# Kernel optimization log

Measured on AMD Instinct MI355X. Metric: run time of the kernel, lower is better.

Reference implementation:

```python
import jax, jax.numpy as jnp
import numpy as np

B = 512        # graphs per batch
N_NODES = 64   # nodes per graph
IN_CH = 256
EMBED = 64
TOPK = 20
NEG_SLOPE = 0.2


def setup_inputs() -> dict:
    key = jax.random.key(0)
    ks = jax.random.split(key, 6)
    N = B * N_NODES
    x = jax.random.normal(ks[0], (N, IN_CH), dtype=jnp.float32)
    # fully-connected graph WITH self loops, per graph, sorted source-major
    src = jnp.repeat(jnp.arange(N_NODES, dtype=jnp.int32), N_NODES)  # [n*n]
    dst = jnp.tile(jnp.arange(N_NODES, dtype=jnp.int32), N_NODES)    # [n*n]
    offs = (jnp.arange(B, dtype=jnp.int32) * N_NODES)[:, None]       # [B,1]
    l = (src[None, :] + offs).reshape(-1)
    r = (dst[None, :] + offs).reshape(-1)
    edge_index = jnp.stack([l, r]).astype(jnp.int32)                 # [2, B*n*n]
    batch = jnp.repeat(jnp.arange(B, dtype=jnp.int32), N_NODES)      # [N]
    glorot = lambda k, sh: jax.random.uniform(k, sh, jnp.float32,
                                              -1.0, 1.0) * np.sqrt(6.0 / (sh[0] + sh[-1]))
    Wl = glorot(ks[1], (EMBED, IN_CH))
    bl = jnp.zeros((EMBED,), jnp.float32)
    Wr = glorot(ks[2], (EMBED, IN_CH))
    br = jnp.zeros((EMBED,), jnp.float32)
    att = glorot(ks[3], (1, EMBED))
    return {"x": x, "edge_index": edge_index, "batch": batch,
            "Wl": Wl, "bl": bl, "Wr": Wr, "br": br, "att": att}


def reference(x, edge_index, batch, Wl, bl, Wr, br, att):
    N = x.shape[0]
    x_l = x @ Wl.T + bl                      # [N, D]
    x_r = x @ Wr.T + br                      # [N, D]
    l, r = edge_index[0], edge_index[1]
    # edge gather + GAT-style score
    e = jax.nn.leaky_relu(x_l[l] + x_r[r], negative_slope=NEG_SLOPE)  # [E, D]
    alpha = (e * att[0]).sum(axis=-1)                                  # [E]
    # segment softmax grouped by source node l (each group is non-empty)
    m = jax.ops.segment_max(alpha, l, num_segments=N)
    a = jnp.exp(alpha - m[l])
    s = jax.ops.segment_sum(a, l, num_segments=N)
    a = a / s[l]
    # kNN sparsify: zero the diagonal then per-row topk
    a3 = a.reshape(B, N_NODES, N_NODES)
    a3 = a3 * (1.0 - jnp.eye(N_NODES, dtype=a3.dtype))
    attention, indices = jax.lax.top_k(a3, TOPK)     # [B, n, k] sorted desc
    attention = attention.reshape(-1)                 # [B*n*k]
    offs = (jnp.arange(B, dtype=jnp.int32) * N_NODES)[:, None]
    index_i = (jnp.repeat(jnp.arange(N_NODES, dtype=jnp.int32), TOPK)[None, :]
               + offs).reshape(-1)
    index_j = (indices.astype(jnp.int32)
               + (jnp.arange(B, dtype=jnp.int32) * N_NODES)[:, None, None]).reshape(-1)
    new_edge_index = jnp.stack([index_i, index_j])    # [2, B*n*k]
    return new_edge_index, attention
```

## Files before the change

kernel.cpp:

```cpp
#include <hip/hip_runtime.h>
#include <stdint.h>

#define NGRAPH 512
#define NN 64
#define INCH 256
#define TOPK 20
#define EPR 655360

typedef __attribute__((ext_vector_type(8))) short bf16x8;
typedef __attribute__((ext_vector_type(4))) float f32x4;

#define STG   0
#define XLF   0
#define XRF   4352
#define ALF   8704
#define SLOF  13056
#define SROF  13120
#define ATTO  13184
#define SMEM_DW 13248

static __device__ __forceinline__ uint32_t f2bfbits(float f) {
  uint32_t u = __float_as_uint(f);
  return (u + 0x7FFFu + ((u >> 16) & 1u)) >> 16;
}
static __device__ __forceinline__ uint32_t pk2(float a, float b) {
  return f2bfbits(a) | (f2bfbits(b) << 16);
}

__global__ __launch_bounds__(256) void wpack(const float* __restrict__ Wl,
                                             const float* __restrict__ Wr,
                                             uint32_t* __restrict__ ws) {
  const int t = blockIdx.x * 256 + threadIdx.x;
  const float* src = (t < 8192) ? Wl : Wr;
  const int p = t & 8191;
  float2 v = *(const float2*)(src + (size_t)p * 2);
  ws[t] = pk2(v.x, v.y);
}

__global__ __launch_bounds__(1024, 8) void gat_fused(
    const float* __restrict__ x,
    const uint32_t* __restrict__ ws,
    const float* __restrict__ blv,
    const float* __restrict__ brv,
    const float* __restrict__ att,
    float* __restrict__ out)
{
  __shared__ __align__(16) uint32_t smemU[SMEM_DW];
  float* smemF = (float*)smemU;

  const int b    = blockIdx.x;
  const int t    = threadIdx.x;
  const int w    = t >> 6;
  const int lane = t & 63;
  const int quad = lane >> 4;
  const int lo   = lane & 15;
  const int nodeBase = b * NN;

  if (t < 64) smemF[ATTO + t] = att[t];

  const int half = w >> 3;
  const int r0   = ((w >> 1) & 3) * 16;
  const int kh   = w & 1;
  const int pair = w >> 1;

  f32x4 acc[4];
  #pragma unroll
  for (int ct = 0; ct < 4; ++ct) acc[ct] = (f32x4){0.f, 0.f, 0.f, 0.f};

  const uint4* wsV = (const uint4*)ws;
  #pragma unroll
  for (int ksl = 0; ksl < 4; ++ksl) {
    const int ks = kh * 4 + ksl;
    const int k0 = ks * 32 + quad * 8;
    const float* ap = x + (size_t)(nodeBase + r0 + lo) * INCH + k0;
    float4 a0 = *(const float4*)ap;
    float4 a1 = *(const float4*)(ap + 4);
    uint4 au = { pk2(a0.x, a0.y), pk2(a0.z, a0.w), pk2(a1.x, a1.y), pk2(a1.z, a1.w) };
    bf16x8 afrag = __builtin_bit_cast(bf16x8, au);
    #pragma unroll
    for (int ct = 0; ct < 4; ++ct) {
      const int n = ct * 16 + lo;
      uint4 bu = wsV[half * 2048 + n * 32 + ks * 4 + quad];
      bf16x8 bfrag = __builtin_bit_cast(bf16x8, bu);
      acc[ct] = __builtin_amdgcn_mfma_f32_16x16x32_bf16(afrag, bfrag, acc[ct], 0, 0, 0);
    }
  }

  if (kh) {
    #pragma unroll
    for (int ct = 0; ct < 4; ++ct)
      *(f32x4*)&smemF[STG + pair * 1280 + (ct * 16 + lo) * 20 + quad * 4] = acc[ct];
  }
  __syncthreads();

  f32x4 vfin[4];
  if (!kh) {
    const float* bias = half ? brv : blv;
    #pragma unroll
    for (int ct = 0; ct < 4; ++ct) {
      f32x4 pv = *(const f32x4*)&smemF[STG + pair * 1280 + (ct * 16 + lo) * 20 + quad * 4];
      const float bb = bias[ct * 16 + lo];
      vfin[ct][0] = acc[ct][0] + pv[0] + bb;
      vfin[ct][1] = acc[ct][1] + pv[1] + bb;
      vfin[ct][2] = acc[ct][2] + pv[2] + bb;
      vfin[ct][3] = acc[ct][3] + pv[3] + bb;
    }
  }
  __syncthreads();
  if (!kh) {
    const int dstBase = half ? XRF : XLF;
    #pragma unroll
    for (int ct = 0; ct < 4; ++ct)
      *(f32x4*)&smemF[dstBase + (ct * 16 + lo) * 68 + r0 + quad * 4] = vfin[ct];
  }
  __syncthreads();

  {
    const int idx = t >> 3;
    const int seg = t & 7;
    const int i = idx & 63;
    const int srcB = (idx < 64) ? XLF : XRF;
    float s = 0.f;
    #pragma unroll
    for (int dd = 0; dd < 8; ++dd) {
      const int d = dd * 8 + seg;
      s = fmaf(smemF[ATTO + d], smemF[srcB + d * 68 + i], s);
    }
    s += __shfl_xor(s, 1);
    s += __shfl_xor(s, 2);
    s += __shfl_xor(s, 4);
    if (seg == 0) smemF[((idx < 64) ? SLOF : SROF) + i] = s;
  }
  __syncthreads();

  {
    const int i0 = t >> 4;
    const int j0 = (t & 15) * 4;
    float pacc[4] = {0.f, 0.f, 0.f, 0.f};
    #pragma unroll 4
    for (int d = 0; d < 64; ++d) {
      const float xl0 = smemF[XLF + d * 68 + i0];
      const f32x4 xr  = *(const f32x4*)&smemF[XRF + d * 68 + j0];
      const float ad  = smemF[ATTO + d];
      #pragma unroll
      for (int c = 0; c < 4; ++c) {
        const float s0 = xl0 + xr[c];
        pacc[c] = fmaf(ad, fabsf(s0), pacc[c]);
      }
    }
    const float sl = smemF[SLOF + i0];
    const f32x4 srv = *(const f32x4*)&smemF[SROF + j0];
    f32x4 v;
    #pragma unroll
    for (int c = 0; c < 4; ++c)
      v[c] = 0.6f * (sl + srv[c]) + 0.4f * pacc[c];
    *(f32x4*)&smemF[ALF + i0 * 68 + j0] = v;
  }
  __syncthreads();

  {
    const int rB = w * 4;
    float aq[4], mq[4], Sq[4];
    uint32_t key[4];
    #pragma unroll
    for (int q = 0; q < 4; ++q)
      aq[q] = smemF[ALF + (rB + q) * 68 + lane];

    #pragma unroll
    for (int q = 0; q < 4; ++q) mq[q] = aq[q];
    #pragma unroll
    for (int msk = 32; msk >= 1; msk >>= 1)
      #pragma unroll
      for (int q = 0; q < 4; ++q)
        mq[q] = fmaxf(mq[q], __shfl_xor(mq[q], msk));

    #pragma unroll
    for (int q = 0; q < 4; ++q) Sq[q] = __expf(aq[q] - mq[q]);
    #pragma unroll
    for (int msk = 32; msk >= 1; msk >>= 1)
      #pragma unroll
      for (int q = 0; q < 4; ++q)
        Sq[q] += __shfl_xor(Sq[q], msk);

    #pragma unroll
    for (int q = 0; q < 4; ++q) {
      const uint32_t u = __float_as_uint(aq[q]);
      uint32_t kk = u ^ ((uint32_t)((int32_t)u >> 31) | 0x80000000u);
      kk = (kk & 0xFFFFFFC0u) | (uint32_t)(63 - lane);
      key[q] = (lane == rB + q) ? 0u : kk;
    }

    #pragma unroll
    for (int k = 2; k <= 64; k <<= 1) {
      #pragma unroll
      for (int j = k >> 1; j >= 1; j >>= 1) {
        const bool keep_max = (((lane & k) == 0) == ((lane & j) == 0));
        #pragma unroll
        for (int q = 0; q < 4; ++q) {
          const uint32_t p = __shfl_xor(key[q], j);
          const uint32_t mx = (key[q] > p) ? key[q] : p;
          const uint32_t mn = (key[q] > p) ? p : key[q];
          key[q] = keep_max ? mx : mn;
        }
      }
    }

    if (lane < TOPK) {
      #pragma unroll
      for (int q = 0; q < 4; ++q) {
        const int g = nodeBase + rB + q;
        const uint32_t kq = key[q];
        const uint32_t ub = (kq & 0x80000000u) ? (kq ^ 0x80000000u) : ~kq;
        const float alpha = __uint_as_float(ub & 0xFFFFFFC0u);
        const int jj = 63 - (int)(kq & 63u);
        const float va = __expf(alpha - mq[q]) * (1.0f / Sq[q]);
        out[(size_t)g * 20 + lane] = (float)g;
        out[(size_t)EPR + (size_t)g * 20 + lane] = (float)(nodeBase + jj);
        out[2 * (size_t)EPR + (size_t)g * 20 + lane] = va;
      }
    }
  }
}

extern "C" void kernel_launch(void* const* d_in, const int* in_sizes, int n_in,
                              void* d_out, int out_size, void* d_ws, size_t ws_size,
                              hipStream_t stream) {
  const float* x   = (const float*)d_in[0];
  const float* Wl  = (const float*)d_in[3];
  const float* bl  = (const float*)d_in[4];
  const float* Wr  = (const float*)d_in[5];
  const float* br  = (const float*)d_in[6];
  const float* att = (const float*)d_in[7];
  uint32_t* wsW = (uint32_t*)d_ws;

  wpack<<<dim3(64), dim3(256), 0, stream>>>(Wl, Wr, wsW);
  gat_fused<<<dim3(NGRAPH), dim3(1024), 0, stream>>>(x, wsW, bl, br, att, (float*)d_out);
}
```

Measured before the change: 130.9 us.

## Fuse score, softmax and top-k per wave using readlane and DPP

```diff
diff --git a/kernel.cpp b/kernel.cpp
--- a/kernel.cpp
+++ b/kernel.cpp
@@ -11,13 +11,9 @@
 typedef __attribute__((ext_vector_type(4))) float f32x4;
 
 #define STG   0
-#define XLF   0
-#define XRF   4352
-#define ALF   8704
-#define SLOF  13056
-#define SROF  13120
-#define ATTO  13184
-#define SMEM_DW 13248
+#define XLR   0
+#define XRR   4352
+#define SMEM_DW 10240
 
 static __device__ __forceinline__ uint32_t f2bfbits(float f) {
   uint32_t u = __float_as_uint(f);
@@ -25,6 +21,24 @@
 }
 static __device__ __forceinline__ uint32_t pk2(float a, float b) {
   return f2bfbits(a) | (f2bfbits(b) << 16);
+}
+
+static __device__ __forceinline__ float keyalpha(uint32_t k) {
+  uint32_t ub = (k & 0x80000000u) ? (k ^ 0x80000000u) : ~k;
+  return __uint_as_float(ub & 0xFFFFFFC0u);
+}
+
+static __device__ __forceinline__ float redsum64(float v) {
+  int p;
+  p = __builtin_amdgcn_update_dpp(0, __float_as_int(v), 0xB1, 0xF, 0xF, true);
+  v += __int_as_float(p);
+  p = __builtin_amdgcn_update_dpp(0, __float_as_int(v), 0x4E, 0xF, 0xF, true);
+  v += __int_as_float(p);
+  v += __shfl_xor(v, 4);
+  v += __shfl_xor(v, 8);
+  v += __shfl_xor(v, 16);
+  v += __shfl_xor(v, 32);
+  return v;
 }
 
 __global__ __launch_bounds__(256) void wpack(const float* __restrict__ Wl,
@@ -56,8 +70,6 @@
   const int lo   = lane & 15;
   const int nodeBase = b * NN;
 
-  if (t < 64) smemF[ATTO + t] = att[t];
-
   const int half = w >> 3;
   const int r0   = ((w >> 1) & 3) * 16;
   const int kh   = w & 1;
@@ -108,116 +120,120 @@
   }
   __syncthreads();
   if (!kh) {
-    const int dstBase = half ? XRF : XLF;
-    #pragma unroll
-    for (int ct = 0; ct < 4; ++ct)
-      *(f32x4*)&smemF[dstBase + (ct * 16 + lo) * 68 + r0 + quad * 4] = vfin[ct];
+    if (half == 0) {
+      #pragma unroll
+      for (int ct = 0; ct < 4; ++ct)
+        #pragma unroll
+        for (int rg = 0; rg < 4; ++rg)
+          smemF[XLR + (r0 + quad * 4 + rg) * 68 + ct * 16 + lo] = vfin[ct][rg];
+    } else {
+      #pragma unroll
+      for (int ct = 0; ct < 4; ++ct)
+        #pragma unroll
+        for (int rg = 0; rg < 4; ++rg) {
+          const int row = r0 + quad * 4 + rg;
+          const int dsw = (ct * 16 + lo) ^ ((row & 7) << 2);
+          smemF[XRR + row * 64 + dsw] = vfin[ct][rg];
+        }
+    }
   }
   __syncthreads();
 
-  {
-    const int idx = t >> 3;
-    const int seg = t & 7;
-    const int i = idx & 63;
-    const int srcB = (idx < 64) ? XLF : XRF;
-    float s = 0.f;
-    #pragma unroll
-    for (int dd = 0; dd < 8; ++dd) {
-      const int d = dd * 8 + seg;
-      s = fmaf(smemF[ATTO + d], smemF[srcB + d * 68 + i], s);
-    }
-    s += __shfl_xor(s, 1);
-    s += __shfl_xor(s, 2);
-    s += __shfl_xor(s, 4);
-    if (seg == 0) smemF[((idx < 64) ? SLOF : SROF) + i] = s;
-  }
-  __syncthreads();
-
-  {
-    const int i0 = t >> 4;
-    const int j0 = (t & 15) * 4;
-    float pacc[4] = {0.f, 0.f, 0.f, 0.f};
-    #pragma unroll 4
-    for (int d = 0; d < 64; ++d) {
-      const float xl0 = smemF[XLF + d * 68 + i0];
-      const f32x4 xr  = *(const f32x4*)&smemF[XRF + d * 68 + j0];
-      const float ad  = smemF[ATTO + d];
-      #pragma unroll
-      for (int c = 0; c < 4; ++c) {
-        const float s0 = xl0 + xr[c];
-        pacc[c] = fmaf(ad, fabsf(s0), pacc[c]);
+  const int rB = w * 4;
+
+  float xlv[4];
+  #pragma unroll
+  for (int q = 0; q < 4; ++q)
+    xlv[q] = smemF[XLR + (rB + q) * 68 + lane];
+
+  const float attv = att[lane];
+  float sl[4];
+  #pragma unroll
+  for (int q = 0; q < 4; ++q)
+    sl[q] = redsum64(attv * xlv[q]);
+
+  float pacc[4] = {0.f, 0.f, 0.f, 0.f};
+  float srp = 0.f;
+  const int xrb = XRR + lane * 64;
+  const int sw  = lane & 7;
+  #pragma unroll
+  for (int c = 0; c < 4; ++c) {
+    f32x4 xrc[4];
+    #pragma unroll
+    for (int g = 0; g < 4; ++g)
+      xrc[g] = *(const f32x4*)&smemF[xrb + (((c * 4 + g) ^ sw) << 2)];
+    #pragma unroll
+    for (int dl = 0; dl < 16; ++dl) {
+      const int d = c * 16 + dl;
+      const float xv = xrc[dl >> 2][dl & 3];
+      const float av = att[d];
+      srp = fmaf(av, xv, srp);
+      #pragma unroll
+      for (int q = 0; q < 4; ++q) {
+        const float xls = __int_as_float(
+            __builtin_amdgcn_readlane(__float_as_int(xlv[q]), d));
+        pacc[q] = fmaf(av, fabsf(xls + xv), pacc[q]);
       }
     }
-    const float sl = smemF[SLOF + i0];
-    const f32x4 srv = *(const f32x4*)&smemF[SROF + j0];
-    f32x4 v;
-    #pragma unroll
-    for (int c = 0; c < 4; ++c)
-      v[c] = 0.6f * (sl + srv[c]) + 0.4f * pacc[c];
-    *(f32x4*)&smemF[ALF + i0 * 68 + j0] = v;
-  }
-  __syncthreads();
-
-  {
-    const int rB = w * 4;
-    float aq[4], mq[4], Sq[4];
-    uint32_t key[4];
-    #pragma unroll
-    for (int q = 0; q < 4; ++q)
-      aq[q] = smemF[ALF + (rB + q) * 68 + lane];
-
-    #pragma unroll
-    for (int q = 0; q < 4; ++q) mq[q] = aq[q];
-    #pragma unroll
-    for (int msk = 32; msk >= 1; msk >>= 1)
-      #pragma unroll
-      for (int q = 0; q < 4; ++q)
-        mq[q] = fmaxf(mq[q], __shfl_xor(mq[q], msk));
-
-    #pragma unroll
-    for (int q = 0; q < 4; ++q) Sq[q] = __expf(aq[q] - mq[q]);
-    #pragma unroll
-    for (int msk = 32; msk >= 1; msk >>= 1)
-      #pragma unroll
-      for (int q = 0; q < 4; ++q)
-        Sq[q] += __shfl_xor(Sq[q], msk);
-
+  }
+
+  float aq[4];
+  #pragma unroll
+  for (int q = 0; q < 4; ++q)
+    aq[q] = 0.6f * (sl[q] + srp) + 0.4f * pacc[q];
+
+  uint32_t key[4];
+  #pragma unroll
+  for (int q = 0; q < 4; ++q) {
+    const uint32_t u = __float_as_uint(aq[q]);
+    uint32_t kk = u ^ ((uint32_t)((int32_t)u >> 31) | 0x80000000u);
+    kk = (kk & 0xFFFFFFC0u) | (uint32_t)(63 - lane);
+    key[q] = (lane == rB + q) ? 0u : kk;
+  }
+
+  #pragma unroll
+  for (int k = 2; k <= 64; k <<= 1) {
+    #pragma unroll
+    for (int j = k >> 1; j >= 1; j >>= 1) {
+      const bool keep_max = (((lane & k) == 0) == ((lane & j) == 0));
+      #pragma unroll
+      for (int q = 0; q < 4; ++q) {
+        uint32_t p;
+        if (j == 1)
+          p = (uint32_t)__builtin_amdgcn_update_dpp(0, (int)key[q], 0xB1, 0xF, 0xF, true);
+        else if (j == 2)
+          p = (uint32_t)__builtin_amdgcn_update_dpp(0, (int)key[q], 0x4E, 0xF, 0xF, true);
+        else
+          p = (uint32_t)__shfl_xor((int)key[q], j);
+        const uint32_t mx = (key[q] > p) ? key[q] : p;
+        const uint32_t mn = (key[q] > p) ? p : key[q];
+        key[q] = keep_max ? mx : mn;
+      }
+    }
+  }
+
+  float mq[4], Sq[4];
+  #pragma unroll
+  for (int q = 0; q < 4; ++q) {
+    const uint32_t tk = (uint32_t)__builtin_amdgcn_readlane((int)key[q], 0);
+    const float topa  = keyalpha(tk);
+    const float adiag = __int_as_float(
+        __builtin_amdgcn_readlane(__float_as_int(aq[q]), rB + q));
+    mq[q] = fmaxf(topa, adiag);
+    Sq[q] = redsum64(__expf(aq[q] - mq[q]));
+  }
+
+  if (lane < TOPK) {
     #pragma unroll
     for (int q = 0; q < 4; ++q) {
-      const uint32_t u = __float_as_uint(aq[q]);
-      uint32_t kk = u ^ ((uint32_t)((int32_t)u >> 31) | 0x80000000u);
-      kk = (kk & 0xFFFFFFC0u) | (uint32_t)(63 - lane);
-      key[q] = (lane == rB + q) ? 0u : kk;
-    }
-
-    #pragma unroll
-    for (int k = 2; k <= 64; k <<= 1) {
-      #pragma unroll
-      for (int j = k >> 1; j >= 1; j >>= 1) {
-        const bool keep_max = (((lane & k) == 0) == ((lane & j) == 0));
-        #pragma unroll
-        for (int q = 0; q < 4; ++q) {
-          const uint32_t p = __shfl_xor(key[q], j);
-          const uint32_t mx = (key[q] > p) ? key[q] : p;
-          const uint32_t mn = (key[q] > p) ? p : key[q];
-          key[q] = keep_max ? mx : mn;
-        }
-      }
-    }
-
-    if (lane < TOPK) {
-      #pragma unroll
-      for (int q = 0; q < 4; ++q) {
-        const int g = nodeBase + rB + q;
-        const uint32_t kq = key[q];
-        const uint32_t ub = (kq & 0x80000000u) ? (kq ^ 0x80000000u) : ~kq;
-        const float alpha = __uint_as_float(ub & 0xFFFFFFC0u);
-        const int jj = 63 - (int)(kq & 63u);
-        const float va = __expf(alpha - mq[q]) * (1.0f / Sq[q]);
-        out[(size_t)g * 20 + lane] = (float)g;
-        out[(size_t)EPR + (size_t)g * 20 + lane] = (float)(nodeBase + jj);
-        out[2 * (size_t)EPR + (size_t)g * 20 + lane] = va;
-      }
+      const int g = nodeBase + rB + q;
+      const uint32_t kq = key[q];
+      const float alpha = keyalpha(kq);
+      const int jj = 63 - (int)(kq & 63u);
+      const float va = __expf(alpha - mq[q]) * (1.0f / Sq[q]);
+      out[(size_t)g * 20 + lane] = (float)g;
+      out[(size_t)EPR + (size_t)g * 20 + lane] = (float)(nodeBase + jj);
+      out[2 * (size_t)EPR + (size_t)g * 20 + lane] = va;
     }
   }
 }
```

Result: no change. 130.6 us (-0.2%).
